# Kernel optimization log

Hardware: AMD Instinct MI355X
Metric: run time of the kernel (lower is better)

Reference implementation:

```python
import jax, jax.numpy as jnp
import numpy as np

DIM = 128
BATCH = 262144
N_PAIRS = DIM * (DIM - 1) // 2  # 8128

# Static pair ordering exactly as in the torch module: (i, j) for i in range(dim) for j in range(i+1, dim)
_p = np.array([(i, j) for i in range(DIM) for j in range(i + 1, DIM)], dtype=np.int32)
I_IDX = jnp.asarray(_p[:, 0])
J_IDX = jnp.asarray(_p[:, 1])


def setup_inputs() -> dict:
    key = jax.random.key(0)
    k1, k2 = jax.random.split(key)
    x = jax.random.normal(k1, (BATCH, DIM), dtype=jnp.float32)
    angles = jax.random.normal(k2, (N_PAIRS,), dtype=jnp.float32) * 0.01
    bias = jnp.zeros((DIM,), dtype=jnp.float32)
    return {"x": x, "angles": angles, "bias": bias}


def _rotation_matrix(angles):
    # The layer is linear: applying the ordered Givens sweep to every row of x
    # equals x @ W where W is the sweep applied to eye(dim) (cf. weight_matrix()).
    # Building W via a scan over the 8128 rotations is the efficient faithful form.
    cos, sin = jnp.cos(angles), jnp.sin(angles)

    def step(W, vals):
        i, j, c, s = vals
        wi = W[:, i]  # [dim]
        wj = W[:, j]
        # out[:, [i,j]] @ [[c, -s], [s, c]]  ->  new_i = wi*c + wj*s ; new_j = wj*c - wi*s
        W = W.at[:, i].set(wi * c + wj * s)
        W = W.at[:, j].set(wj * c - wi * s)
        return W, None

    W0 = jnp.eye(DIM, dtype=angles.dtype)
    W, _ = jax.lax.scan(step, W0, (I_IDX, J_IDX, cos, sin))
    return W


def reference(x, angles, bias):
    W = _rotation_matrix(angles)  # [dim, dim] orthogonal
    return x @ W + bias
```

## Files before the change

kernel.cpp:

```cpp
#include <hip/hip_runtime.h>

typedef float  floatx4  __attribute__((ext_vector_type(4)));
typedef short  bf16x8   __attribute__((ext_vector_type(8)));
typedef float  facc4    __attribute__((ext_vector_type(4)));

__device__ __forceinline__ unsigned short f2bf(float f) {
  unsigned u = __builtin_bit_cast(unsigned, f);
  u = u + 0x7fffu + ((u >> 16) & 1u);
  return (unsigned short)(u >> 16);
}

template <int I0, int I1>
__device__ void gen_chunk(const float* __restrict__ ang, float* __restrict__ out,
                          float* lcs, int tid) {
  constexpr int P0 = I0 * 127 - I0 * (I0 - 1) / 2;
  constexpr int P1 = I1 * 127 - I1 * (I1 - 1) / 2;
  constexpr int NROT = P1 - P0;
  for (int idx = tid; idx < NROT; idx += 256) {
    float s, c;
    sincosf(ang[P0 + idx], &s, &c);
    lcs[2 * idx] = c;
    lcs[2 * idx + 1] = s;
  }
  __syncthreads();
  if (tid >= 128) return;
  float w[128];
#pragma unroll
  for (int k = 0; k < 128; ++k) w[k] = (k == tid) ? 1.0f : 0.0f;
#pragma unroll
  for (int i = I0; i < I1; ++i) {
    float wi = w[i];
#pragma unroll
    for (int j = i + 1; j < 128; ++j) {
      const int p = (i * 127 - (i * (i - 1)) / 2 + (j - i - 1)) - P0;
      const float2 cs2 = *(const float2*)(&lcs[2 * p]);
      const float c = cs2.x, s = cs2.y;
      const float wj = w[j];
      w[j] = fmaf(wj, c, -(wi * s));
      wi   = fmaf(wj, s, wi * c);
    }
    w[i] = wi;
  }
  floatx4* o = (floatx4*)(out + (size_t)tid * 128);
#pragma unroll
  for (int k = 0; k < 32; ++k) {
    floatx4 v;
    v[0] = w[4 * k]; v[1] = w[4 * k + 1]; v[2] = w[4 * k + 2]; v[3] = w[4 * k + 3];
    o[k] = v;
  }
}

__global__ __launch_bounds__(256) void k_wgen(const float* __restrict__ ang,
                                              float* __restrict__ out) {
  __shared__ float lcs[2144];
  const int tid = threadIdx.x;
  switch (blockIdx.x) {
    case 0:  gen_chunk<0,   8>(ang, out + 0 * 16384, lcs, tid); break;
    case 1:  gen_chunk<8,  17>(ang, out + 1 * 16384, lcs, tid); break;
    case 2:  gen_chunk<17, 27>(ang, out + 2 * 16384, lcs, tid); break;
    case 3:  gen_chunk<27, 37>(ang, out + 3 * 16384, lcs, tid); break;
    case 4:  gen_chunk<37, 49>(ang, out + 4 * 16384, lcs, tid); break;
    case 5:  gen_chunk<49, 64>(ang, out + 5 * 16384, lcs, tid); break;
    case 6:  gen_chunk<64, 82>(ang, out + 6 * 16384, lcs, tid); break;
    default: gen_chunk<82, 127>(ang, out + 7 * 16384, lcs, tid); break;
  }
}

__global__ __launch_bounds__(128) void k_combine(const float* __restrict__ chunks,
                                                 unsigned short* __restrict__ wt) {
  __shared__ float sv[128];
  const int r = blockIdx.x;
  const int t = threadIdx.x;
  float v = chunks[r * 128 + t];
  for (int m = 1; m < 8; ++m) {
    __syncthreads();
    sv[t] = v;
    __syncthreads();
    const float* Cm = chunks + m * 16384 + t;
    float a0 = 0.f, a1 = 0.f, a2 = 0.f, a3 = 0.f;
#pragma unroll
    for (int k = 0; k < 128; k += 4) {
      a0 = fmaf(sv[k],     Cm[(k)     * 128], a0);
      a1 = fmaf(sv[k + 1], Cm[(k + 1) * 128], a1);
      a2 = fmaf(sv[k + 2], Cm[(k + 2) * 128], a2);
      a3 = fmaf(sv[k + 3], Cm[(k + 3) * 128], a3);
    }
    v = (a0 + a1) + (a2 + a3);
  }
  wt[t * 136 + r] = f2bf(v);
}

__global__ __launch_bounds__(256) void k_gemm(const float* __restrict__ x,
                                              const unsigned short* __restrict__ wt,
                                              const float* __restrict__ bias,
                                              float* __restrict__ y) {
  __shared__ unsigned short sW[128 * 136];
  __shared__ float sB[128];
  const int tid = threadIdx.x;
  {
    const floatx4* src = (const floatx4*)wt;
    floatx4* dst = (floatx4*)sW;
#pragma unroll
    for (int i2 = 0; i2 < 9; ++i2) {
      int idx = tid + i2 * 256;
      if (idx < 2176) dst[idx] = src[idx];
    }
    if (tid < 128) sB[tid] = bias[tid];
  }
  __syncthreads();

  const int wave = tid >> 6, lane = tid & 63;
  const int m16 = lane & 15, h = lane >> 4;

  const size_t row0 = (size_t)blockIdx.x * 256 + wave * 64 + m16;
  const float* xr0 = x + row0 * 128;
  float* yr0 = y + row0 * 128;

  floatx4 a[8];
#pragma unroll
  for (int c = 0; c < 4; ++c) {
    a[2 * c]     = *(const floatx4*)(xr0 + c * 32 + h * 8);
    a[2 * c + 1] = *(const floatx4*)(xr0 + c * 32 + h * 8 + 4);
  }

#pragma unroll
  for (int it = 0; it < 4; ++it) {
    bf16x8 af[4];
#pragma unroll
    for (int c = 0; c < 4; ++c) {
#pragma unroll
      for (int q = 0; q < 8; ++q) {
        const float f = (q < 4) ? a[2 * c][q] : a[2 * c + 1][q - 4];
        af[c][q] = (short)f2bf(f);
      }
    }
    if (it < 3) {
      const float* xr = xr0 + (size_t)(it + 1) * 16 * 128;
#pragma unroll
      for (int c = 0; c < 4; ++c) {
        a[2 * c]     = *(const floatx4*)(xr + c * 32 + h * 8);
        a[2 * c + 1] = *(const floatx4*)(xr + c * 32 + h * 8 + 4);
      }
    }
    facc4 acc[8];
#pragma unroll
    for (int t = 0; t < 8; ++t) acc[t] = *(const facc4*)(sB + t * 16 + h * 4);
#pragma unroll
    for (int c = 0; c < 4; ++c) {
#pragma unroll
      for (int t = 0; t < 8; ++t) {
        const bf16x8 bw = *(const bf16x8*)(&sW[(t * 16 + m16) * 136 + c * 32 + h * 8]);
        acc[t] = __builtin_amdgcn_mfma_f32_16x16x32_bf16(bw, af[c], acc[t], 0, 0, 0);
      }
    }
    float* yr = yr0 + (size_t)it * 16 * 128;
#pragma unroll
    for (int t = 0; t < 8; ++t) {
      *(floatx4*)(yr + t * 16 + h * 4) = acc[t];
    }
  }
}

extern "C" void kernel_launch(void* const* d_in, const int* in_sizes, int n_in,
                              void* d_out, int out_size, void* d_ws, size_t ws_size,
                              hipStream_t stream) {
  const float* x    = (const float*)d_in[0];
  const float* ang  = (const float*)d_in[1];
  const float* bias = (const float*)d_in[2];
  float* y = (float*)d_out;

  char* ws = (char*)d_ws;
  float* chunks      = (float*)ws;
  unsigned short* wt = (unsigned short*)(ws + 524288);

  k_wgen   <<<8,    256, 0, stream>>>(ang, chunks);
  k_combine<<<128,  128, 0, stream>>>(chunks, wt);
  k_gemm   <<<1024, 256, 0, stream>>>(x, wt, bias, y);
}
```

Measured before the change: 288.3 us.

## Rework W generation into LDS, swizzle GEMM weights, double-buffer x loads

The W generator now keeps each thread's row in shared memory instead of a fully unrolled register array. It splits the rotations into 9 chunks with runtime bounds and a 128-thread block, and the combine kernel multiplies one extra chunk. The GEMM stores W in LDS with an XOR swizzle instead of padding, prefetches two row-tiles of x ahead, writes output with nontemporal stores, and sets an occupancy hint. Together these aim to shorten the serial W-generation prologue and reduce LDS bank conflicts and memory stalls in the bandwidth-bound GEMM, at the cost of more registers for the prefetch buffers.

Result: slower. 421.8 us (+46.3%).

```diff
diff --git a/kernel.cpp b/kernel.cpp
--- a/kernel.cpp
+++ b/kernel.cpp
@@ -10,59 +10,44 @@
   return (unsigned short)(u >> 16);
 }
 
-template <int I0, int I1>
-__device__ void gen_chunk(const float* __restrict__ ang, float* __restrict__ out,
-                          float* lcs, int tid) {
-  constexpr int P0 = I0 * 127 - I0 * (I0 - 1) / 2;
-  constexpr int P1 = I1 * 127 - I1 * (I1 - 1) / 2;
-  constexpr int NROT = P1 - P0;
-  for (int idx = tid; idx < NROT; idx += 256) {
+__device__ const int kBounds[10] = {0, 7, 15, 23, 32, 42, 54, 67, 85, 127};
+
+__global__ __launch_bounds__(128) void k_wgen(const float* __restrict__ ang,
+                                              float* __restrict__ out) {
+  __shared__ float  lw[128 * 129];
+  __shared__ float2 lcs[960];
+  const int tid = threadIdx.x;
+  const int I0 = kBounds[blockIdx.x], I1 = kBounds[blockIdx.x + 1];
+  const int P0 = I0 * 127 - (I0 * (I0 - 1)) / 2;
+  const int P1 = I1 * 127 - (I1 * (I1 - 1)) / 2;
+  const int nrot = P1 - P0;
+
+  for (int p = tid; p < nrot; p += 128) {
     float s, c;
-    sincosf(ang[P0 + idx], &s, &c);
-    lcs[2 * idx] = c;
-    lcs[2 * idx + 1] = s;
+    sincosf(ang[P0 + p], &s, &c);
+    lcs[p].x = c;
+    lcs[p].y = s;
+  }
+  float* wr = lw + tid * 129;
+  for (int c = 0; c < 128; ++c) wr[c] = 0.0f;
+  wr[tid] = 1.0f;
+  __syncthreads();
+
+  int p = 0;
+  for (int i = I0; i < I1; ++i) {
+    float wi = wr[i];
+    for (int j = i + 1; j < 128; ++j, ++p) {
+      const float2 cs2 = lcs[p];
+      const float wj = wr[j];
+      wr[j] = fmaf(wj, cs2.x, -(wi * cs2.y));
+      wi    = fmaf(wj, cs2.y, wi * cs2.x);
+    }
+    wr[i] = wi;
   }
   __syncthreads();
-  if (tid >= 128) return;
-  float w[128];
-#pragma unroll
-  for (int k = 0; k < 128; ++k) w[k] = (k == tid) ? 1.0f : 0.0f;
-#pragma unroll
-  for (int i = I0; i < I1; ++i) {
-    float wi = w[i];
-#pragma unroll
-    for (int j = i + 1; j < 128; ++j) {
-      const int p = (i * 127 - (i * (i - 1)) / 2 + (j - i - 1)) - P0;
-      const float2 cs2 = *(const float2*)(&lcs[2 * p]);
-      const float c = cs2.x, s = cs2.y;
-      const float wj = w[j];
-      w[j] = fmaf(wj, c, -(wi * s));
-      wi   = fmaf(wj, s, wi * c);
-    }
-    w[i] = wi;
-  }
-  floatx4* o = (floatx4*)(out + (size_t)tid * 128);
-#pragma unroll
-  for (int k = 0; k < 32; ++k) {
-    floatx4 v;
-    v[0] = w[4 * k]; v[1] = w[4 * k + 1]; v[2] = w[4 * k + 2]; v[3] = w[4 * k + 3];
-    o[k] = v;
-  }
-}
-
-__global__ __launch_bounds__(256) void k_wgen(const float* __restrict__ ang,
-                                              float* __restrict__ out) {
-  __shared__ float lcs[2144];
-  const int tid = threadIdx.x;
-  switch (blockIdx.x) {
-    case 0:  gen_chunk<0,   8>(ang, out + 0 * 16384, lcs, tid); break;
-    case 1:  gen_chunk<8,  17>(ang, out + 1 * 16384, lcs, tid); break;
-    case 2:  gen_chunk<17, 27>(ang, out + 2 * 16384, lcs, tid); break;
-    case 3:  gen_chunk<27, 37>(ang, out + 3 * 16384, lcs, tid); break;
-    case 4:  gen_chunk<37, 49>(ang, out + 4 * 16384, lcs, tid); break;
-    case 5:  gen_chunk<49, 64>(ang, out + 5 * 16384, lcs, tid); break;
-    case 6:  gen_chunk<64, 82>(ang, out + 6 * 16384, lcs, tid); break;
-    default: gen_chunk<82, 127>(ang, out + 7 * 16384, lcs, tid); break;
+  float* dst = out + (size_t)blockIdx.x * 16384;
+  for (int e = tid; e < 16384; e += 128) {
+    dst[e] = lw[(e >> 7) * 129 + (e & 127)];
   }
 }
 
@@ -72,7 +57,7 @@
   const int r = blockIdx.x;
   const int t = threadIdx.x;
   float v = chunks[r * 128 + t];
-  for (int m = 1; m < 8; ++m) {
+  for (int m = 1; m < 9; ++m) {
     __syncthreads();
     sv[t] = v;
     __syncthreads();
@@ -87,23 +72,24 @@
     }
     v = (a0 + a1) + (a2 + a3);
   }
-  wt[t * 136 + r] = f2bf(v);
+  wt[t * 128 + r] = f2bf(v);
 }
 
-__global__ __launch_bounds__(256) void k_gemm(const float* __restrict__ x,
-                                              const unsigned short* __restrict__ wt,
-                                              const float* __restrict__ bias,
-                                              float* __restrict__ y) {
-  __shared__ unsigned short sW[128 * 136];
+__global__ __launch_bounds__(256, 4) void k_gemm(const float* __restrict__ x,
+                                                 const unsigned short* __restrict__ wt,
+                                                 const float* __restrict__ bias,
+                                                 float* __restrict__ y) {
+  __shared__ unsigned short sW[128 * 128];
   __shared__ float sB[128];
   const int tid = threadIdx.x;
   {
     const floatx4* src = (const floatx4*)wt;
     floatx4* dst = (floatx4*)sW;
 #pragma unroll
-    for (int i2 = 0; i2 < 9; ++i2) {
-      int idx = tid + i2 * 256;
-      if (idx < 2176) dst[idx] = src[idx];
+    for (int i2 = 0; i2 < 8; ++i2) {
+      const int idx = tid + i2 * 256;
+      const int row = idx >> 4, ch = idx & 15;
+      dst[(row << 4) | (ch ^ (row & 15))] = src[idx];
     }
     if (tid < 128) sB[tid] = bias[tid];
   }
@@ -113,33 +99,39 @@
   const int m16 = lane & 15, h = lane >> 4;
 
   const size_t row0 = (size_t)blockIdx.x * 256 + wave * 64 + m16;
-  const float* xr0 = x + row0 * 128;
-  float* yr0 = y + row0 * 128;
+  const float* xw = x + row0 * 128 + h * 8;
+  float* yw = y + row0 * 128;
 
-  floatx4 a[8];
+  floatx4 a[2][8];
 #pragma unroll
   for (int c = 0; c < 4; ++c) {
-    a[2 * c]     = *(const floatx4*)(xr0 + c * 32 + h * 8);
-    a[2 * c + 1] = *(const floatx4*)(xr0 + c * 32 + h * 8 + 4);
+    a[0][2 * c]     = *(const floatx4*)(xw + c * 32);
+    a[0][2 * c + 1] = *(const floatx4*)(xw + c * 32 + 4);
+  }
+#pragma unroll
+  for (int c = 0; c < 4; ++c) {
+    a[1][2 * c]     = *(const floatx4*)(xw + 2048 + c * 32);
+    a[1][2 * c + 1] = *(const floatx4*)(xw + 2048 + c * 32 + 4);
   }
 
 #pragma unroll
   for (int it = 0; it < 4; ++it) {
+    const int cur = it & 1;
     bf16x8 af[4];
 #pragma unroll
     for (int c = 0; c < 4; ++c) {
 #pragma unroll
       for (int q = 0; q < 8; ++q) {
-        const float f = (q < 4) ? a[2 * c][q] : a[2 * c + 1][q - 4];
+        const float f = (q < 4) ? a[cur][2 * c][q] : a[cur][2 * c + 1][q - 4];
         af[c][q] = (short)f2bf(f);
       }
     }
-    if (it < 3) {
-      const float* xr = xr0 + (size_t)(it + 1) * 16 * 128;
+    if (it < 2) {
+      const float* xp = xw + (size_t)(it + 2) * 2048;
 #pragma unroll
       for (int c = 0; c < 4; ++c) {
-        a[2 * c]     = *(const floatx4*)(xr + c * 32 + h * 8);
-        a[2 * c + 1] = *(const floatx4*)(xr + c * 32 + h * 8 + 4);
+        a[cur][2 * c]     = *(const floatx4*)(xp + c * 32);
+        a[cur][2 * c + 1] = *(const floatx4*)(xp + c * 32 + 4);
       }
     }
     facc4 acc[8];
@@ -149,14 +141,16 @@
     for (int c = 0; c < 4; ++c) {
 #pragma unroll
       for (int t = 0; t < 8; ++t) {
-        const bf16x8 bw = *(const bf16x8*)(&sW[(t * 16 + m16) * 136 + c * 32 + h * 8]);
+        const int row = t * 16 + m16;
+        const bf16x8 bw =
+            *(const bf16x8*)(sW + (((row << 4) | (((c << 2) | h) ^ m16)) << 3));
         acc[t] = __builtin_amdgcn_mfma_f32_16x16x32_bf16(bw, af[c], acc[t], 0, 0, 0);
       }
     }
-    float* yr = yr0 + (size_t)it * 16 * 128;
+    float* yr = yw + it * 2048;
 #pragma unroll
     for (int t = 0; t < 8; ++t) {
-      *(floatx4*)(yr + t * 16 + h * 4) = acc[t];
+      __builtin_nontemporal_store(acc[t], (floatx4*)(yr + t * 16 + h * 4));
     }
   }
 }
@@ -171,9 +165,9 @@
 
   char* ws = (char*)d_ws;
   float* chunks      = (float*)ws;
-  unsigned short* wt = (unsigned short*)(ws + 524288);
+  unsigned short* wt = (unsigned short*)(ws + 589824);
 
-  k_wgen   <<<8,    256, 0, stream>>>(ang, chunks);
+  k_wgen   <<<9,    128, 0, stream>>>(ang, chunks);
   k_combine<<<128,  128, 0, stream>>>(chunks, wt);
   k_gemm   <<<1024, 256, 0, stream>>>(x, wt, bias, y);
 }
```
